# Performance work log

Hardware: AMD Instinct MI355X
Metric: run time of the kernel (lower is better)

Reference implementation:

```python
import jax, jax.numpy as jnp
import numpy as np

B, T, K = 512, 512, 64


def setup_inputs() -> dict:
    key = jax.random.key(0)
    k1, k2, k3, k4, k5 = jax.random.split(key, 5)
    emissions = jax.random.normal(k1, (B, T, K), dtype=jnp.float32)
    tags = jax.random.randint(k2, (B, T), 0, K)
    mask = jnp.ones((B, T), dtype=bool)  # torchcrf requires mask[:, 0] to be on
    # torchcrf initializes CRF params ~ U(-0.1, 0.1)
    start_transitions = jax.random.uniform(k3, (K,), minval=-0.1, maxval=0.1, dtype=jnp.float32)
    end_transitions = jax.random.uniform(k4, (K,), minval=-0.1, maxval=0.1, dtype=jnp.float32)
    transitions = jax.random.uniform(k5, (K, K), minval=-0.1, maxval=0.1, dtype=jnp.float32)
    return {"emissions": emissions, "tags": tags, "mask": mask,
            "start_transitions": start_transitions,
            "end_transitions": end_transitions,
            "transitions": transitions}


def _crf_nll(emissions, tags, mask, start_transitions, end_transitions, transitions):
    # emissions [B,T,K], tags [B,T] int, mask [B,T] bool
    b, t, k = emissions.shape
    maskf = mask.astype(emissions.dtype)
    batch = jnp.arange(b)

    # ---- numerator: score of the gold tag sequence ----
    em = jnp.take_along_axis(emissions, tags[:, :, None], axis=2)[:, :, 0]  # [B,T]
    score = start_transitions[tags[:, 0]] + em[:, 0]
    tr_sc = transitions[tags[:, :-1], tags[:, 1:]]  # [B,T-1]
    score = score + jnp.sum((tr_sc + em[:, 1:]) * maskf[:, 1:], axis=1)
    seq_ends = jnp.sum(mask.astype(jnp.int32), axis=1) - 1  # [B]
    last_tags = tags[batch, seq_ends]
    score = score + end_transitions[last_tags]

    # ---- denominator: log-partition via forward algorithm (scan over time) ----
    alpha0 = start_transitions[None, :] + emissions[:, 0]  # [B,K]

    def step(alpha, inp):
        em_t, m_t = inp  # [B,K], [B]
        # [B, prev K, next K] -> logsumexp over prev
        nxt = jax.nn.logsumexp(alpha[:, :, None] + transitions[None, :, :] + em_t[:, None, :], axis=1)
        alpha = jnp.where(m_t[:, None], nxt, alpha)
        return alpha, None

    em_rest = jnp.swapaxes(emissions[:, 1:], 0, 1)  # [T-1,B,K]
    m_rest = jnp.swapaxes(mask[:, 1:], 0, 1)        # [T-1,B]
    alphaT, _ = jax.lax.scan(step, alpha0, (em_rest, m_rest))
    denom = jax.nn.logsumexp(alphaT + end_transitions[None, :], axis=1)  # [B]

    llh = score - denom  # [B]
    return -jnp.mean(llh)  # reduction='mean', loss = -llh


def reference(emissions, tags, mask, start_transitions, end_transitions, transitions):
    return _crf_nll(emissions, tags, mask, start_transitions, end_transitions, transitions)
```

## Files before the change

### kernel.cpp

```cpp
#include <hip/hip_runtime.h>

#define KK 64
#define TT 512
#define BB 512
#define NW (BB / 32)
#define LOG2E 1.44269504088896340736f
#define LN2 0.69314718055994530942f

typedef float f32x16 __attribute__((ext_vector_type(16)));
typedef float f32x4v __attribute__((ext_vector_type(4)));
typedef int i32x4 __attribute__((ext_vector_type(4)));
typedef short bf16x8 __attribute__((ext_vector_type(8)));

__global__ __launch_bounds__(64) void crf_score(
    const float* __restrict__ em, const int* __restrict__ tags,
    const float* __restrict__ start, const float* __restrict__ endt,
    const float* __restrict__ trans, float* __restrict__ score_out)
{
  const int b = blockIdx.x;
  const int lane = threadIdx.x;
  const int* tg = tags + b * TT;
  const float* e = em + (size_t)b * TT * KK;
  float s = 0.f;
#pragma unroll
  for (int rep = 0; rep < TT / 64; ++rep) {
    int t = rep * 64 + lane;
    int cur = tg[t];
    s += e[t * KK + cur];
    if (t > 0) s += trans[tg[t - 1] * KK + cur];
  }
#pragma unroll
  for (int off = 32; off; off >>= 1) s += __shfl_xor(s, off);
  if (lane == 0) {
    s += start[tg[0]] + endt[tg[TT - 1]];
    score_out[b] = s;
  }
}

__global__ __launch_bounds__(256) void crf_wexp(const float* __restrict__ em,
                                                float* __restrict__ wout)
{
  int tid = blockIdx.x * 256 + threadIdx.x;
  int l = tid & 63;
  int i = (tid >> 6) & 7;
  int t = (tid >> 9) & 511;
  int cw = tid >> 18;
  int b = cw * 32 + (l & 31);
  int jb = (i >> 2) * 32 + (i & 3) * 8 + (l >> 5) * 4;
  f32x4v e = *(const f32x4v*)(em + ((size_t)b * TT + t) * KK + jb);
  f32x4v w;
  w[0] = exp2f(e[0] * LOG2E);
  w[1] = exp2f(e[1] * LOG2E);
  w[2] = exp2f(e[2] * LOG2E);
  w[3] = exp2f(e[3] * LOG2E);
  ((f32x4v*)wout)[tid] = w;
}


#define XR(kt, q) ((kt) < 2 ? x0[((kt)&1) * 8 + (q)] : x1[((kt)&1) * 8 + (q)])

#define LOADW(WBUF, TN)                                                        \
  {                                                                            \
    int tn_ = (TN) < TT ? (TN) : (TT - 1);                                     \
    if (USEW) {                                                                \
      _Pragma("unroll") for (int i2 = 0; i2 < 8; ++i2)                         \
          WBUF[i2] = wb_base[((size_t)tn_ * 8 + i2) * 64 + lane];              \
    } else {                                                                   \
      _Pragma("unroll") for (int i2 = 0; i2 < 8; ++i2)                         \
          WBUF[i2] = *(const f32x4v*)(em_b + (size_t)tn_ * KK +                \
                                      (i2 >> 2) * 32 + (i2 & 3) * 8 + hi * 4);\
    }                                                                          \
  }

#define STEP(WBUF, TNEXT, RENORM)                                              \
  {                                                                            \
    f32x16 d0 = {};                                                            \
    f32x16 d1 = {};                                                            \
    _Pragma("unroll") for (int kt = 0; kt < 4; ++kt)                           \
    {                                                                          \
      bf16x8 bfv = __builtin_bit_cast(bf16x8, st[kt]);                         \
      d0 = __builtin_amdgcn_mfma_f32_32x32x16_bf16(afr[0][kt], bfv, d0, 0, 0, 0);\
      d1 = __builtin_amdgcn_mfma_f32_32x32x16_bf16(afr[1][kt], bfv, d1, 0, 0, 0);\
    }                                                                          \
    f32x16 x0, x1;                                                             \
    if (USEW) {                                                                \
      _Pragma("unroll") for (int q = 0; q < 16; ++q)                           \
      {                                                                        \
        x0[q] = d0[q] * WBUF[q >> 2][q & 3];                                   \
        x1[q] = d1[q] * WBUF[4 + (q >> 2)][q & 3];                             \
      }                                                                        \
    } else {                                                                   \
      _Pragma("unroll") for (int q = 0; q < 16; ++q)                           \
      {                                                                        \
        x0[q] = d0[q] * exp2f(WBUF[q >> 2][q & 3] * LOG2E);                    \
        x1[q] = d1[q] * exp2f(WBUF[4 + (q >> 2)][q & 3] * LOG2E);              \
      }                                                                        \
    }                                                                          \
    if (RENORM) {                                                              \
      float m_ = x0[0];                                                        \
      float px_ = m_, py_ = m_;                                                \
      asm("v_permlane32_swap_b32 %0, %1" : "+v"(px_), "+v"(py_));              \
      float pm_ = (lane & 32) ? py_ : px_;                                     \
      float mm_ = fmaxf(m_, pm_);                                              \
      int ee_ = (int)(__float_as_uint(mm_) >> 23) - 127;                       \
      S2 += (float)ee_;                                                        \
      _Pragma("unroll") for (int q = 0; q < 16; ++q)                           \
      {                                                                        \
        x0[q] = ldexpf(x0[q], -ee_);                                           \
        x1[q] = ldexpf(x1[q], -ee_);                                           \
      }                                                                        \
    }                                                                          \
    LOADW(WBUF, TNEXT)                                                         \
    _Pragma("unroll") for (int kt = 0; kt < 4; ++kt)                           \
    {                                                                          \
      int P0, P1, P2, P3;                                                      \
      asm("v_cvt_pk_bf16_f32 %0, %1, %2" : "=v"(P0) : "v"(XR(kt, 0)), "v"(XR(kt, 1)));\
      asm("v_cvt_pk_bf16_f32 %0, %1, %2" : "=v"(P1) : "v"(XR(kt, 2)), "v"(XR(kt, 3)));\
      asm("v_cvt_pk_bf16_f32 %0, %1, %2" : "=v"(P2) : "v"(XR(kt, 4)), "v"(XR(kt, 5)));\
      asm("v_cvt_pk_bf16_f32 %0, %1, %2" : "=v"(P3) : "v"(XR(kt, 6)), "v"(XR(kt, 7)));\
      asm("v_permlane32_swap_b32 %0, %1" : "+v"(P2), "+v"(P0));                \
      asm("v_permlane32_swap_b32 %0, %1" : "+v"(P3), "+v"(P1));                \
      st[kt] = (i32x4){P0, P1, P2, P3};                                        \
    }                                                                          \
  }

template <bool USEW>
__global__ __attribute__((amdgpu_flat_work_group_size(64, 64),
                          amdgpu_waves_per_eu(1, 1)))
void crf_forward_mfma(const float* __restrict__ em,
                      const float* __restrict__ start,
                      const float* __restrict__ endt,
                      const float* __restrict__ trans,
                      const float* __restrict__ wtab,
                      float* __restrict__ denom_out)
{
  const int cw = blockIdx.x;
  const int lane = threadIdx.x;
  const int lo = lane & 31;
  const int hi = lane >> 5;
  const int b = cw * 32 + lo;
  const float* em_b = em + (size_t)b * TT * KK;
  const f32x4v* wb_base = (const f32x4v*)wtab + (size_t)cw * TT * 8 * 64;

  bf16x8 afr[2][4];
#pragma unroll
  for (int rt = 0; rt < 2; ++rt)
#pragma unroll
    for (int kt = 0; kt < 4; ++kt) {
      int pw[4];
#pragma unroll
      for (int p = 0; p < 4; ++p) {
        int k0 = kt * 16 + hi * 8 + 2 * p;
        float e0 = exp2f(trans[k0 * KK + rt * 32 + lo] * LOG2E);
        float e1 = exp2f(trans[(k0 + 1) * KK + rt * 32 + lo] * LOG2E);
        asm("v_cvt_pk_bf16_f32 %0, %1, %2" : "=v"(pw[p]) : "v"(e0), "v"(e1));
      }
      afr[rt][kt] = __builtin_bit_cast(bf16x8, (i32x4){pw[0], pw[1], pw[2], pw[3]});
    }

  i32x4 st[4];
#pragma unroll
  for (int kt = 0; kt < 4; ++kt) {
    int pw[4];
#pragma unroll
    for (int p = 0; p < 4; ++p) {
      int j0 = kt * 16 + hi * 8 + 2 * p;
      float v0 = exp2f((start[j0] + em_b[j0]) * LOG2E);
      float v1 = exp2f((start[j0 + 1] + em_b[j0 + 1]) * LOG2E);
      asm("v_cvt_pk_bf16_f32 %0, %1, %2" : "=v"(pw[p]) : "v"(v0), "v"(v1));
    }
    st[kt] = (i32x4){pw[0], pw[1], pw[2], pw[3]};
  }

  float S2 = 0.f;
  f32x4v wA[8], wB[8], wC[8];
  LOADW(wA, 1)
  LOADW(wB, 2)
  LOADW(wC, 3)

  int tb = 1;
  for (int it = 0; it < 170; ++it) {
    STEP(wA, tb + 3, false)
    STEP(wB, tb + 4, false)
    STEP(wC, tb + 5, true)
    tb += 3;
  }
  STEP(wA, TT - 1, false)

  float sum = 0.f;
#pragma unroll
  for (int kt = 0; kt < 4; ++kt)
#pragma unroll
    for (int f = 0; f < 4; ++f) {
      int w = st[kt][f];
      int j0 = kt * 16 + hi * 8 + 2 * f;
      float vlo = __uint_as_float(((unsigned)w) << 16);
      float vhi = __uint_as_float(((unsigned)w) & 0xffff0000u);
      sum += vlo * exp2f(endt[j0] * LOG2E) + vhi * exp2f(endt[j0 + 1] * LOG2E);
    }
  float total = sum + __shfl_xor(sum, 32);
  if (lane < 32) denom_out[cw * 32 + lane] = (log2f(total) + S2) * LN2;
}

__global__ __launch_bounds__(512) void crf_final(
    const float* __restrict__ score, const float* __restrict__ denom,
    float* __restrict__ out)
{
  const int i = threadIdx.x;
  float d = denom[i] - score[i];
  __shared__ float red[8];
#pragma unroll
  for (int off = 32; off; off >>= 1) d += __shfl_xor(d, off);
  if ((i & 63) == 0) red[i >> 6] = d;
  __syncthreads();
  if (i == 0) {
    float s = 0.f;
#pragma unroll
    for (int wv = 0; wv < 8; ++wv) s += red[wv];
    out[0] = s / (float)BB;
  }
}

extern "C" void kernel_launch(void* const* d_in, const int* in_sizes, int n_in,
                              void* d_out, int out_size, void* d_ws, size_t ws_size,
                              hipStream_t stream) {
  const float* em = (const float*)d_in[0];
  const int* tags = (const int*)d_in[1];
  const float* start = (const float*)d_in[3];
  const float* endt = (const float*)d_in[4];
  const float* trans = (const float*)d_in[5];

  float* score = (float*)d_ws;
  float* denom = score + BB;
  float* wtab = (float*)((char*)d_ws + 8192);
  const size_t wbytes = (size_t)NW * TT * 8 * 64 * 16;

  crf_score<<<BB, 64, 0, stream>>>(em, tags, start, endt, trans, score);
  if (ws_size >= 8192 + wbytes) {
    crf_wexp<<<(NW * TT * 8 * 64) / 256, 256, 0, stream>>>(em, wtab);
    crf_forward_mfma<true><<<NW, 64, 0, stream>>>(em, start, endt, trans, wtab, denom);
  } else {
    crf_forward_mfma<false><<<NW, 64, 0, stream>>>(em, start, endt, trans, nullptr, denom);
  }
  crf_final<<<1, BB, 0, stream>>>(score, denom, (float*)d_out);
}
```

Measured before the change: 198.6 us.

## Interleave two independent batch chains per wave in CRF forward MFMA kernel

The forward-recurrence kernel now has each wave process two 32-sequence batch groups, so it launches half as many single-wave blocks. The MFMAs and elementwise work of the two chains are interleaved, which gives the scheduler four independent accumulators per step to hide MFMA and conversion latency along the serial time recurrence. In exchange each step issues twice the MFMA and VALU work on one wave, and register use roughly doubles (six prefetch buffers plus a per-lane end-transition table), which risks spills. The fallback path without the workspace table no longer applies the exponential to the emissions.

```diff
diff --git a/kernel.cpp b/kernel.cpp
--- a/kernel.cpp
+++ b/kernel.cpp
@@ -4,6 +4,7 @@
 #define TT 512
 #define BB 512
 #define NW (BB / 32)
+#define NB2 (NW / 2)
 #define LOG2E 1.44269504088896340736f
 #define LN2 0.69314718055994530942f
 
@@ -11,6 +12,8 @@
 typedef float f32x4v __attribute__((ext_vector_type(4)));
 typedef int i32x4 __attribute__((ext_vector_type(4)));
 typedef short bf16x8 __attribute__((ext_vector_type(8)));
+
+#define MF(A, B, C) __builtin_amdgcn_mfma_f32_32x32x16_bf16((A), (B), (C), 0, 0, 0)
 
 __global__ __launch_bounds__(64) void crf_score(
     const float* __restrict__ em, const int* __restrict__ tags,
@@ -57,90 +60,114 @@
 }
 
 
-#define XR(kt, q) ((kt) < 2 ? x0[((kt)&1) * 8 + (q)] : x1[((kt)&1) * 8 + (q)])
-
-#define LOADW(WBUF, TN)                                                        \
+#define XR2(X0, X1, kt, q) ((kt) < 2 ? X0[((kt)&1) * 8 + (q)] : X1[((kt)&1) * 8 + (q)])
+
+#define CVTSW(ST, X0, X1)                                                      \
+  _Pragma("unroll") for (int kt = 0; kt < 4; ++kt)                             \
+  {                                                                            \
+    int P0, P1, P2, P3;                                                        \
+    asm("v_cvt_pk_bf16_f32 %0, %1, %2" : "=v"(P0) : "v"(XR2(X0, X1, kt, 0)), "v"(XR2(X0, X1, kt, 1))); \
+    asm("v_cvt_pk_bf16_f32 %0, %1, %2" : "=v"(P1) : "v"(XR2(X0, X1, kt, 2)), "v"(XR2(X0, X1, kt, 3))); \
+    asm("v_cvt_pk_bf16_f32 %0, %1, %2" : "=v"(P2) : "v"(XR2(X0, X1, kt, 4)), "v"(XR2(X0, X1, kt, 5))); \
+    asm("v_cvt_pk_bf16_f32 %0, %1, %2" : "=v"(P3) : "v"(XR2(X0, X1, kt, 6)), "v"(XR2(X0, X1, kt, 7))); \
+    asm("v_permlane32_swap_b32 %0, %1" : "+v"(P2), "+v"(P0));                  \
+    asm("v_permlane32_swap_b32 %0, %1" : "+v"(P3), "+v"(P1));                  \
+    ST[kt] = (i32x4){P0, P1, P2, P3};                                          \
+  }
+
+#define LOADW2(WBUF, TN, WBASE, EMB)                                           \
   {                                                                            \
     int tn_ = (TN) < TT ? (TN) : (TT - 1);                                     \
     if (USEW) {                                                                \
       _Pragma("unroll") for (int i2 = 0; i2 < 8; ++i2)                         \
-          WBUF[i2] = wb_base[((size_t)tn_ * 8 + i2) * 64 + lane];              \
+          WBUF[i2] = WBASE[((size_t)tn_ * 8 + i2) * 64 + lane];                \
     } else {                                                                   \
       _Pragma("unroll") for (int i2 = 0; i2 < 8; ++i2)                         \
-          WBUF[i2] = *(const f32x4v*)(em_b + (size_t)tn_ * KK +                \
+          WBUF[i2] = *(const f32x4v*)(EMB + (size_t)tn_ * KK +                 \
                                       (i2 >> 2) * 32 + (i2 & 3) * 8 + hi * 4);\
     }                                                                          \
   }
 
-#define STEP(WBUF, TNEXT, RENORM)                                              \
-  {                                                                            \
-    f32x16 d0 = {};                                                            \
-    f32x16 d1 = {};                                                            \
+#define RENORM1(X0, X1, S2V)                                                   \
+  {                                                                            \
+    float m_ = X0[0];                                                          \
+    float pm_ = __shfl_xor(m_, 32);                                            \
+    float mm_ = fmaxf(m_, pm_);                                                \
+    int ee_ = (int)(__float_as_uint(mm_) >> 23) - 127;                         \
+    S2V += (float)ee_;                                                         \
+    _Pragma("unroll") for (int q = 0; q < 16; ++q)                             \
+    {                                                                          \
+      X0[q] = ldexpf(X0[q], -ee_);                                             \
+      X1[q] = ldexpf(X1[q], -ee_);                                             \
+    }                                                                          \
+  }
+
+#define STEP2(WA, WB, TN, RENORM)                                              \
+  {                                                                            \
+    f32x16 dA0 = {}; f32x16 dA1 = {}; f32x16 dB0 = {}; f32x16 dB1 = {};        \
     _Pragma("unroll") for (int kt = 0; kt < 4; ++kt)                           \
     {                                                                          \
-      bf16x8 bfv = __builtin_bit_cast(bf16x8, st[kt]);                         \
-      d0 = __builtin_amdgcn_mfma_f32_32x32x16_bf16(afr[0][kt], bfv, d0, 0, 0, 0);\
-      d1 = __builtin_amdgcn_mfma_f32_32x32x16_bf16(afr[1][kt], bfv, d1, 0, 0, 0);\
-    }                                                                          \
-    f32x16 x0, x1;                                                             \
-    if (USEW) {                                                                \
-      _Pragma("unroll") for (int q = 0; q < 16; ++q)                           \
-      {                                                                        \
-        x0[q] = d0[q] * WBUF[q >> 2][q & 3];                                   \
-        x1[q] = d1[q] * WBUF[4 + (q >> 2)][q & 3];                             \
-      }                                                                        \
-    } else {                                                                   \
-      _Pragma("unroll") for (int q = 0; q < 16; ++q)                           \
-      {                                                                        \
-        x0[q] = d0[q] * exp2f(WBUF[q >> 2][q & 3] * LOG2E);                    \
-        x1[q] = d1[q] * exp2f(WBUF[4 + (q >> 2)][q & 3] * LOG2E);              \
-      }                                                                        \
+      bf16x8 va_ = __builtin_bit_cast(bf16x8, stA[kt]);                        \
+      bf16x8 vb_ = __builtin_bit_cast(bf16x8, stB[kt]);                        \
+      dA0 = MF(afr[0][kt], va_, dA0);                                          \
+      dB0 = MF(afr[0][kt], vb_, dB0);                                          \
+      dA1 = MF(afr[1][kt], va_, dA1);                                          \
+      dB1 = MF(afr[1][kt], vb_, dB1);                                          \
+    }                                                                          \
+    f32x16 xA0, xA1, xB0, xB1;                                                 \
+    _Pragma("unroll") for (int q = 0; q < 16; ++q)                             \
+    {                                                                          \
+      xA0[q] = dA0[q] * WA[q >> 2][q & 3];                                     \
+      xB0[q] = dB0[q] * WB[q >> 2][q & 3];                                     \
+      xA1[q] = dA1[q] * WA[4 + (q >> 2)][q & 3];                               \
+      xB1[q] = dB1[q] * WB[4 + (q >> 2)][q & 3];                               \
     }                                                                          \
     if (RENORM) {                                                              \
-      float m_ = x0[0];                                                        \
-      float px_ = m_, py_ = m_;                                                \
-      asm("v_permlane32_swap_b32 %0, %1" : "+v"(px_), "+v"(py_));              \
-      float pm_ = (lane & 32) ? py_ : px_;                                     \
-      float mm_ = fmaxf(m_, pm_);                                              \
-      int ee_ = (int)(__float_as_uint(mm_) >> 23) - 127;                       \
-      S2 += (float)ee_;                                                        \
-      _Pragma("unroll") for (int q = 0; q < 16; ++q)                           \
-      {                                                                        \
-        x0[q] = ldexpf(x0[q], -ee_);                                           \
-        x1[q] = ldexpf(x1[q], -ee_);                                           \
-      }                                                                        \
-    }                                                                          \
-    LOADW(WBUF, TNEXT)                                                         \
+      RENORM1(xA0, xA1, S2A)                                                   \
+      RENORM1(xB0, xB1, S2B)                                                   \
+    }                                                                          \
+    LOADW2(WA, TN, wbA, emA_b)                                                 \
+    LOADW2(WB, TN, wbB, emB_b)                                                 \
+    CVTSW(stA, xA0, xA1)                                                       \
+    CVTSW(stB, xB0, xB1)                                                       \
+  }
+
+#define FINSUM(ST, S2V, CW)                                                    \
+  {                                                                            \
+    float sum_ = 0.f;                                                          \
     _Pragma("unroll") for (int kt = 0; kt < 4; ++kt)                           \
-    {                                                                          \
-      int P0, P1, P2, P3;                                                      \
-      asm("v_cvt_pk_bf16_f32 %0, %1, %2" : "=v"(P0) : "v"(XR(kt, 0)), "v"(XR(kt, 1)));\
-      asm("v_cvt_pk_bf16_f32 %0, %1, %2" : "=v"(P1) : "v"(XR(kt, 2)), "v"(XR(kt, 3)));\
-      asm("v_cvt_pk_bf16_f32 %0, %1, %2" : "=v"(P2) : "v"(XR(kt, 4)), "v"(XR(kt, 5)));\
-      asm("v_cvt_pk_bf16_f32 %0, %1, %2" : "=v"(P3) : "v"(XR(kt, 6)), "v"(XR(kt, 7)));\
-      asm("v_permlane32_swap_b32 %0, %1" : "+v"(P2), "+v"(P0));                \
-      asm("v_permlane32_swap_b32 %0, %1" : "+v"(P3), "+v"(P1));                \
-      st[kt] = (i32x4){P0, P1, P2, P3};                                        \
-    }                                                                          \
+        _Pragma("unroll") for (int f = 0; f < 4; ++f)                          \
+    {                                                                          \
+      int w_ = ST[kt][f];                                                      \
+      int j0_ = kt * 16 + hi * 8 + 2 * f;                                      \
+      float vlo_ = __uint_as_float(((unsigned)w_) << 16);                      \
+      float vhi_ = __uint_as_float(((unsigned)w_) & 0xffff0000u);              \
+      sum_ += vlo_ * eend[j0_] + vhi_ * eend[j0_ + 1];                         \
+    }                                                                          \
+    float total_ = sum_ + __shfl_xor(sum_, 32);                                \
+    if (lane < 32) denom_out[(CW)*32 + lane] = (log2f(total_) + S2V) * LN2;    \
   }
 
 template <bool USEW>
 __global__ __attribute__((amdgpu_flat_work_group_size(64, 64),
                           amdgpu_waves_per_eu(1, 1)))
-void crf_forward_mfma(const float* __restrict__ em,
-                      const float* __restrict__ start,
-                      const float* __restrict__ endt,
-                      const float* __restrict__ trans,
-                      const float* __restrict__ wtab,
-                      float* __restrict__ denom_out)
-{
-  const int cw = blockIdx.x;
+void crf_forward_mfma2(const float* __restrict__ em,
+                       const float* __restrict__ start,
+                       const float* __restrict__ endt,
+                       const float* __restrict__ trans,
+                       const float* __restrict__ wtab,
+                       float* __restrict__ denom_out)
+{
+  const int blk = blockIdx.x;
   const int lane = threadIdx.x;
   const int lo = lane & 31;
   const int hi = lane >> 5;
-  const int b = cw * 32 + lo;
-  const float* em_b = em + (size_t)b * TT * KK;
-  const f32x4v* wb_base = (const f32x4v*)wtab + (size_t)cw * TT * 8 * 64;
+  const int cwA = blk * 2, cwB = blk * 2 + 1;
+  const int bA = cwA * 32 + lo, bB = cwB * 32 + lo;
+  const float* emA_b = em + (size_t)bA * TT * KK;
+  const float* emB_b = em + (size_t)bB * TT * KK;
+  const f32x4v* wbA = (const f32x4v*)wtab + (size_t)cwA * TT * 8 * 64;
+  const f32x4v* wbB = (const f32x4v*)wtab + (size_t)cwB * TT * 8 * 64;
 
   bf16x8 afr[2][4];
 #pragma unroll
@@ -158,48 +185,54 @@
       afr[rt][kt] = __builtin_bit_cast(bf16x8, (i32x4){pw[0], pw[1], pw[2], pw[3]});
     }
 
-  i32x4 st[4];
+  float eend[KK];
+#pragma unroll
+  for (int kt = 0; kt < 4; ++kt)
+#pragma unroll
+    for (int f = 0; f < 4; ++f) {
+      int j0 = kt * 16 + hi * 8 + 2 * f;
+      eend[j0] = exp2f(endt[j0] * LOG2E);
+      eend[j0 + 1] = exp2f(endt[j0 + 1] * LOG2E);
+    }
+
+  i32x4 stA[4], stB[4];
 #pragma unroll
   for (int kt = 0; kt < 4; ++kt) {
-    int pw[4];
+    int pwA[4], pwB[4];
 #pragma unroll
     for (int p = 0; p < 4; ++p) {
       int j0 = kt * 16 + hi * 8 + 2 * p;
-      float v0 = exp2f((start[j0] + em_b[j0]) * LOG2E);
-      float v1 = exp2f((start[j0 + 1] + em_b[j0 + 1]) * LOG2E);
-      asm("v_cvt_pk_bf16_f32 %0, %1, %2" : "=v"(pw[p]) : "v"(v0), "v"(v1));
+      float a0 = exp2f((start[j0] + emA_b[j0]) * LOG2E);
+      float a1 = exp2f((start[j0 + 1] + emA_b[j0 + 1]) * LOG2E);
+      float b0 = exp2f((start[j0] + emB_b[j0]) * LOG2E);
+      float b1 = exp2f((start[j0 + 1] + emB_b[j0 + 1]) * LOG2E);
+      asm("v_cvt_pk_bf16_f32 %0, %1, %2" : "=v"(pwA[p]) : "v"(a0), "v"(a1));
+      asm("v_cvt_pk_bf16_f32 %0, %1, %2" : "=v"(pwB[p]) : "v"(b0), "v"(b1));
     }
-    st[kt] = (i32x4){pw[0], pw[1], pw[2], pw[3]};
-  }
-
-  float S2 = 0.f;
-  f32x4v wA[8], wB[8], wC[8];
-  LOADW(wA, 1)
-  LOADW(wB, 2)
-  LOADW(wC, 3)
+    stA[kt] = (i32x4){pwA[0], pwA[1], pwA[2], pwA[3]};
+    stB[kt] = (i32x4){pwB[0], pwB[1], pwB[2], pwB[3]};
+  }
+
+  float S2A = 0.f, S2B = 0.f;
+  f32x4v wA0[8], wA1[8], wA2[8], wB0[8], wB1[8], wB2[8];
+  LOADW2(wA0, 1, wbA, emA_b)
+  LOADW2(wB0, 1, wbB, emB_b)
+  LOADW2(wA1, 2, wbA, emA_b)
+  LOADW2(wB1, 2, wbB, emB_b)
+  LOADW2(wA2, 3, wbA, emA_b)
+  LOADW2(wB2, 3, wbB, emB_b)
 
   int tb = 1;
   for (int it = 0; it < 170; ++it) {
-    STEP(wA, tb + 3, false)
-    STEP(wB, tb + 4, false)
-    STEP(wC, tb + 5, true)
+    STEP2(wA0, wB0, tb + 3, false)
+    STEP2(wA1, wB1, tb + 4, false)
+    STEP2(wA2, wB2, tb + 5, true)
     tb += 3;
   }
-  STEP(wA, TT - 1, false)
-
-  float sum = 0.f;
-#pragma unroll
-  for (int kt = 0; kt < 4; ++kt)
-#pragma unroll
-    for (int f = 0; f < 4; ++f) {
-      int w = st[kt][f];
-      int j0 = kt * 16 + hi * 8 + 2 * f;
-      float vlo = __uint_as_float(((unsigned)w) << 16);
-      float vhi = __uint_as_float(((unsigned)w) & 0xffff0000u);
-      sum += vlo * exp2f(endt[j0] * LOG2E) + vhi * exp2f(endt[j0 + 1] * LOG2E);
-    }
-  float total = sum + __shfl_xor(sum, 32);
-  if (lane < 32) denom_out[cw * 32 + lane] = (log2f(total) + S2) * LN2;
+  STEP2(wA0, wB0, TT - 1, false)
+
+  FINSUM(stA, S2A, cwA)
+  FINSUM(stB, S2B, cwB)
 }
 
 __global__ __launch_bounds__(512) void crf_final(
@@ -238,9 +271,9 @@
   crf_score<<<BB, 64, 0, stream>>>(em, tags, start, endt, trans, score);
   if (ws_size >= 8192 + wbytes) {
     crf_wexp<<<(NW * TT * 8 * 64) / 256, 256, 0, stream>>>(em, wtab);
-    crf_forward_mfma<true><<<NW, 64, 0, stream>>>(em, start, endt, trans, wtab, denom);
+    crf_forward_mfma2<true><<<NB2, 64, 0, stream>>>(em, start, endt, trans, wtab, denom);
   } else {
-    crf_forward_mfma<false><<<NW, 64, 0, stream>>>(em, start, endt, trans, nullptr, denom);
+    crf_forward_mfma2<false><<<NB2, 64, 0, stream>>>(em, start, endt, trans, nullptr, denom);
   }
   crf_final<<<1, BB, 0, stream>>>(score, denom, (float*)d_out);
 }
```

Result: slower. 341.4 us (+71.9%).
